# Performance work log

Hardware: AMD Instinct MI355X
Metric: run time of the kernel (lower is better)

The kernel has to match this reference:

```python
import jax, jax.numpy as jnp
import numpy as np

HIDDEN = 512
HEADS = 8
HEAD_DIM = HIDDEN // HEADS
INNER = int(HIDDEN * 4.0)
MAX_DIST = 512
LN_EPS = 1e-5


def _layernorm(x, g, b):
    mu = jnp.mean(x, axis=-1, keepdims=True)
    var = jnp.var(x, axis=-1, keepdims=True)
    return (x - mu) * jax.lax.rsqrt(var + LN_EPS) * g + b


def setup_inputs() -> dict:
    key = jax.random.key(0)
    ks = jax.random.split(key, 12)
    B, T = 4, 2048
    s = 0.02
    return {
        "x": jax.random.normal(ks[0], (B, T, HIDDEN), dtype=jnp.float32),
        "w_qkv": jax.random.normal(ks[1], (HIDDEN, 3 * HIDDEN), dtype=jnp.float32) * s,
        "b_qkv": jnp.zeros((3 * HIDDEN,), dtype=jnp.float32),
        "w_out": jax.random.normal(ks[2], (HIDDEN, HIDDEN), dtype=jnp.float32) * s,
        "b_out": jnp.zeros((HIDDEN,), dtype=jnp.float32),
        "ln1_g": jnp.ones((HIDDEN,), dtype=jnp.float32),
        "ln1_b": jnp.zeros((HIDDEN,), dtype=jnp.float32),
        "ln2_g": jnp.ones((HIDDEN,), dtype=jnp.float32),
        "ln2_b": jnp.zeros((HIDDEN,), dtype=jnp.float32),
        "w_mlp1": jax.random.normal(ks[3], (HIDDEN, INNER), dtype=jnp.float32) * s,
        "b_mlp1": jnp.zeros((INNER,), dtype=jnp.float32),
        "w_mlp2": jax.random.normal(ks[4], (INNER, HIDDEN), dtype=jnp.float32) * s,
        "b_mlp2": jnp.zeros((HIDDEN,), dtype=jnp.float32),
        "rel_table": jax.random.normal(ks[5], (2 * MAX_DIST + 1, HEADS), dtype=jnp.float32) * s,
    }


def reference(x, w_qkv, b_qkv, w_out, b_out, ln1_g, ln1_b, ln2_g, ln2_b,
              w_mlp1, b_mlp1, w_mlp2, b_mlp2, rel_table):
    B, T, C = x.shape
    scale = HEAD_DIM ** -0.5
    qkv = x @ w_qkv + b_qkv  # [B,T,3C]
    qkv = qkv.reshape(B, T, 3, HEADS, HEAD_DIM)
    q = qkv[:, :, 0].transpose(0, 2, 1, 3)  # [B,H,T,D]
    k = qkv[:, :, 1].transpose(0, 2, 1, 3)
    v = qkv[:, :, 2].transpose(0, 2, 1, 3)
    logits = jnp.einsum('bhqd,bhkd->bhqk', q, k) * scale
    # relative position bias: clamp(q_pos - k_pos) lookup -> [H,T,T]
    rel = jnp.clip(jnp.arange(T)[:, None] - jnp.arange(T)[None, :], -MAX_DIST, MAX_DIST) + MAX_DIST
    bias = rel_table[rel].transpose(2, 0, 1)  # [H,T,T]
    logits = logits + bias[None]
    attn = jax.nn.softmax(logits, axis=-1)
    out = jnp.einsum('bhqk,bhkd->bhqd', attn, v)
    out = out.transpose(0, 2, 1, 3).reshape(B, T, C)
    out = out @ w_out + b_out
    x = _layernorm(x + out, ln1_g, ln1_b)
    h = jax.nn.gelu(x @ w_mlp1 + b_mlp1, approximate=False)
    mlp_out = h @ w_mlp2 + b_mlp2
    return _layernorm(x + mlp_out, ln2_g, ln2_b)
```

## Files before the change

kernel.cpp:

```cpp
#include <hip/hip_runtime.h>
#include <hip/hip_bf16.h>

using bf16 = __hip_bfloat16;
typedef __attribute__((ext_vector_type(8))) short bf16x8;
typedef __attribute__((ext_vector_type(4))) short bf16x4;
typedef __attribute__((ext_vector_type(4))) float f32x4;

#define HIDDEN 512
#define HEADS 8
#define HDIM 64
#define INNER 2048
#define MAXD 512
#define BB 4
#define TT 2048
#define MM (BB*TT)
#define LOG2E 1.44269504088896340736f

typedef const __attribute__((address_space(1))) unsigned int* gas_u32p;
typedef __attribute__((address_space(3))) unsigned int* las_u32p;

__device__ __forceinline__ void gload_lds16(const void* g, void* l) {
    __builtin_amdgcn_global_load_lds((gas_u32p)g, (las_u32p)l, 16, 0, 0);
}
__device__ __forceinline__ short bfr(float x) {
    return (short)__bfloat16_as_ushort(__float2bfloat16(x));
}

__global__ __launch_bounds__(256) void cast_kernel(const float* __restrict__ in,
                                                   bf16* __restrict__ out) {
    int i = (blockIdx.x * 256 + threadIdx.x) * 4;
    float4 v = *(const float4*)&in[i];
    bf16 o[4] = {__float2bfloat16(v.x), __float2bfloat16(v.y),
                 __float2bfloat16(v.z), __float2bfloat16(v.w)};
    *(bf16x4*)&out[i] = *(bf16x4*)o;
}

__global__ __launch_bounds__(256) void wtrans_kernel(const float* __restrict__ in,
                                                     bf16* __restrict__ out,
                                                     int K, int N) {
    __shared__ float tile[32][33];
    int bx = blockIdx.x;
    int by = blockIdx.y;
    int lx = threadIdx.x & 31, ly = threadIdx.x >> 5;
    #pragma unroll
    for (int i = 0; i < 4; ++i)
        tile[ly + 8*i][lx] = in[(size_t)(by*32 + ly + 8*i) * N + bx*32 + lx];
    __syncthreads();
    #pragma unroll
    for (int i = 0; i < 4; ++i)
        out[(size_t)(bx*32 + ly + 8*i) * K + by*32 + lx] =
            __float2bfloat16(tile[lx][ly + 8*i]);
}

template<int EPI, int BN, int VT, int RESID>
__global__ __launch_bounds__(256) void gemm_kernel(
    const bf16* __restrict__ A, const bf16* __restrict__ BT,
    const float* __restrict__ bias, const float* __restrict__ resid,
    void* __restrict__ C, bf16* __restrict__ vt_out,
    int M, int N, int K)
{
    constexpr int NBF = BN / 32;
    constexpr int BBYTES = BN * 64;
    __shared__ __align__(16) bf16 As[2][128*32];
    __shared__ __align__(16) bf16 Bs[2][BN*32];
    const int tid = threadIdx.x;
    const int wid = tid >> 6;
    const int lane = tid & 63;
    const int lhi = lane >> 4, llo = lane & 15;
    const int m0 = blockIdx.x * 128, n0 = blockIdx.y * BN;
    const int wr = wid >> 1, wc = wid & 1;

    const int srow = tid >> 2, scol = (tid & 3) * 8;
    const bf16* Ap = A + (size_t)(m0 + srow) * K + scol;
    const bf16* Bp = BT + (size_t)(n0 + srow) * K + scol;
    const size_t step64 = (size_t)64 * K;

    f32x4 acc[4][NBF] = {};

    gload_lds16(Ap,          (char*)As + tid*16);
    gload_lds16(Ap + step64, (char*)As + 4096 + tid*16);
    gload_lds16(Bp,          (char*)Bs + tid*16);
    if (BN == 128) gload_lds16(Bp + step64, (char*)Bs + 4096 + tid*16);

    const int NK = K >> 5;
    for (int it = 0; it < NK; ++it) {
        const int p = it & 1;
        __syncthreads();
        if (it + 1 < NK) {
            const int k1 = (it + 1) << 5;
            gload_lds16(Ap + k1,          (char*)As + (p^1)*8192 + tid*16);
            gload_lds16(Ap + k1 + step64, (char*)As + (p^1)*8192 + 4096 + tid*16);
            gload_lds16(Bp + k1,          (char*)Bs + (p^1)*BBYTES + tid*16);
            if (BN == 128) gload_lds16(Bp + k1 + step64, (char*)Bs + (p^1)*BBYTES + 4096 + tid*16);
        }
        bf16x8 af[4], bfrg[NBF];
        #pragma unroll
        for (int ar = 0; ar < 4; ++ar)
            af[ar] = *(const bf16x8*)((const char*)As + p*8192 + (64*wr + 16*ar + llo)*64 + lhi*16);
        #pragma unroll
        for (int bc = 0; bc < NBF; ++bc)
            bfrg[bc] = *(const bf16x8*)((const char*)Bs + p*BBYTES + ((BN/2)*wc + 16*bc + llo)*64 + lhi*16);
        #pragma unroll
        for (int ar = 0; ar < 4; ++ar)
            #pragma unroll
            for (int bc = 0; bc < NBF; ++bc)
                acc[ar][bc] = __builtin_amdgcn_mfma_f32_16x16x32_bf16(
                    af[ar], bfrg[bc], acc[ar][bc], 0, 0, 0);
    }

    if (VT && n0 >= 1024) {
        #pragma unroll
        for (int ar = 0; ar < 4; ++ar) {
            const int row = m0 + 64*wr + 16*ar + 4*lhi;
            const int bq = row >> 11, t0 = row & 2047;
            #pragma unroll
            for (int bc = 0; bc < NBF; ++bc) {
                const int cv = n0 - 1024 + (BN/2)*wc + 16*bc + llo;
                const int h = cv >> 6, d = cv & 63;
                float bv = bias[n0 + (BN/2)*wc + 16*bc + llo];
                bf16x4 pk = {bfr(acc[ar][bc][0] + bv), bfr(acc[ar][bc][1] + bv),
                             bfr(acc[ar][bc][2] + bv), bfr(acc[ar][bc][3] + bv)};
                *(bf16x4*)&vt_out[(((size_t)(bq*8 + h) * 64 + d) << 11) + t0] = pk;
            }
        }
        return;
    }

    #pragma unroll
    for (int ar = 0; ar < 4; ++ar) {
        #pragma unroll
        for (int j = 0; j < 4; ++j) {
            int row = m0 + 64*wr + 16*ar + 4*lhi + j;
            #pragma unroll
            for (int bc = 0; bc < NBF; ++bc) {
                int col = n0 + (BN/2)*wc + 16*bc + llo;
                float v = acc[ar][bc][j] + bias[col];
                if (RESID) v += resid[(size_t)row * N + col];
                if (EPI == 2) {
                    float u = 0.7978845608028654f * (v + 0.044715f * v * v * v);
                    float e = __builtin_amdgcn_exp2f(u * (2.0f * LOG2E));
                    v = v * (1.0f - 1.0f / (1.0f + e));
                }
                if (EPI == 1)
                    ((float*)C)[(size_t)row * N + col] = v;
                else
                    ((bf16*)C)[(size_t)row * N + col] = __float2bfloat16(v);
            }
        }
    }
}

#define PTN (TT + 128)
__global__ __launch_bounds__(512) void attn_kernel(
    const bf16* __restrict__ qkv,
    const bf16* __restrict__ v_t,
    const float* __restrict__ rel_table,
    bf16* __restrict__ attn_out)
{
    __shared__ __align__(16) bf16 Ks[2][64*64];
    __shared__ __align__(16) bf16 Vs[2][64*64];
    __shared__ __align__(16) bf16 Ps[8][16*64];
    __shared__ float PT[PTN];

    const int qt = blockIdx.x, bh = blockIdx.y;
    const int b = bh >> 3, h = bh & 7;
    const int tid = threadIdx.x, wid = tid >> 6, lane = tid & 63;
    const int lhi = lane >> 4, llo = lane & 15;

    const int lo = qt * 128 - (TT - 1);
    for (int i = tid; i < PTN; i += 512) {
        int idx = min(max(i + lo, -MAXD), MAXD) + MAXD;
        PT[i] = rel_table[(size_t)idx * HEADS + h] * LOG2E;
    }

    const int q0w = qt * 128 + wid * 16;
    const int q = q0w + llo;
    bf16x8 bq[2];
    #pragma unroll
    for (int kc = 0; kc < 2; ++kc)
        bq[kc] = *(const bf16x8*)&qkv[(size_t)(b*TT + q) * 1536 + h*64 + kc*32 + lhi*8];

    const int so = tid * 16;
    const int r0 = so >> 7;
    const int c0 = (((so & 127) ^ ((r0 & 7) << 4)) >> 1);
    const bf16* kbase = qkv + (size_t)(b*TT) * 1536 + 512 + h*64;
    const bf16* vbase = v_t + (size_t)bh * 64 * TT;

    float accL = 0.f;
    f32x4 accO[4] = {};
    const int pti = wid*16 + llo + (TT - 1);

    gload_lds16(kbase + (size_t)r0 * 1536 + c0, (char*)Ks + so);
    gload_lds16(vbase + (size_t)r0 * TT + c0,   (char*)Vs + so);

    constexpr int NT = TT / 64;
    for (int kt = 0; kt < NT; ++kt) {
        const int p = kt & 1;
        const int kv0 = kt * 64;
        __syncthreads();
        if (kt + 1 < NT) {
            const int kn = kv0 + 64;
            gload_lds16(kbase + (size_t)(kn + r0) * 1536 + c0, (char*)Ks + (p^1)*8192 + so);
            gload_lds16(vbase + (size_t)r0 * TT + kn + c0,     (char*)Vs + (p^1)*8192 + so);
        }
        const char* Kb = (const char*)Ks + p*8192;
        const char* Vb = (const char*)Vs + p*8192;

        f32x4 s[4];
        __builtin_amdgcn_s_setprio(1);
        #pragma unroll
        for (int f = 0; f < 4; ++f) {
            f32x4 a = {};
            const int rr = 16*f + llo;
            #pragma unroll
            for (int kc = 0; kc < 2; ++kc) {
                bf16x8 ak = *(const bf16x8*)(Kb + rr*128 + (((4*kc + lhi) ^ (rr & 7)) << 4));
                a = __builtin_amdgcn_mfma_f32_16x16x32_bf16(ak, bq[kc], a, 0, 0, 0);
            }
            s[f] = a;
        }
        __builtin_amdgcn_s_setprio(0);

        const int ib = pti - kv0;
        #pragma unroll
        for (int f = 0; f < 4; ++f)
            #pragma unroll
            for (int j = 0; j < 4; ++j)
                s[f][j] = s[f][j] * (0.125f * LOG2E) + PT[ib - 16*f - 4*lhi - j];
        float tf[4];
        #pragma unroll
        for (int f = 0; f < 4; ++f) {
            float p0 = __builtin_amdgcn_exp2f(s[f][0]);
            float p1 = __builtin_amdgcn_exp2f(s[f][1]);
            float p2 = __builtin_amdgcn_exp2f(s[f][2]);
            float p3 = __builtin_amdgcn_exp2f(s[f][3]);
            tf[f] = (p0 + p1) + (p2 + p3);
            bf16x4 pk = {bfr(p0), bfr(p1), bfr(p2), bfr(p3)};
            *(bf16x4*)((char*)Ps + wid*2048 + llo*128 +
                       ((f*32 + lhi*8) ^ ((llo & 7) << 4))) = pk;
        }
        accL += (tf[0] + tf[1]) + (tf[2] + tf[3]);

        bf16x8 pf[2];
        #pragma unroll
        for (int kc = 0; kc < 2; ++kc)
            pf[kc] = *(const bf16x8*)((const char*)Ps + wid*2048 + llo*128 +
                                      ((kc*64 + lhi*16) ^ ((llo & 7) << 4)));
        __builtin_amdgcn_s_setprio(1);
        #pragma unroll
        for (int kc = 0; kc < 2; ++kc)
            #pragma unroll
            for (int f = 0; f < 4; ++f) {
                const int rr = 16*f + llo;
                bf16x8 av = *(const bf16x8*)(Vb + rr*128 + (((4*kc + lhi) ^ (rr & 7)) << 4));
                accO[f] = __builtin_amdgcn_mfma_f32_16x16x32_bf16(av, pf[kc], accO[f], 0, 0, 0);
            }
        __builtin_amdgcn_s_setprio(0);
    }

    accL += __shfl_xor(accL, 16, 64);
    accL += __shfl_xor(accL, 32, 64);
    const float rl = 1.0f / accL;
    const int row = b*TT + q;
    #pragma unroll
    for (int f = 0; f < 4; ++f) {
        bf16x4 ov = {bfr(accO[f][0] * rl), bfr(accO[f][1] * rl),
                     bfr(accO[f][2] * rl), bfr(accO[f][3] * rl)};
        *(bf16x4*)&attn_out[(size_t)row * HIDDEN + h*64 + 16*f + 4*lhi] = ov;
    }
}

template<int WB>
__global__ __launch_bounds__(256) void ln_kernel(
    const float* __restrict__ in,
    const float* __restrict__ g, const float* __restrict__ bb,
    float* __restrict__ of, bf16* __restrict__ ob)
{
    int row = blockIdx.x * 4 + (threadIdx.x >> 6);
    int lane = threadIdx.x & 63;
    const float* pa = in + (size_t)row * HIDDEN;
    float v[8];
    float s = 0.f, sq = 0.f;
    #pragma unroll
    for (int i = 0; i < 2; ++i) {
        float4 a4 = *(const float4*)&pa[lane*4 + i*256];
        v[i*4+0] = a4.x; v[i*4+1] = a4.y; v[i*4+2] = a4.z; v[i*4+3] = a4.w;
        #pragma unroll
        for (int j = 0; j < 4; ++j) { s += v[i*4+j]; sq += v[i*4+j]*v[i*4+j]; }
    }
    #pragma unroll
    for (int d = 1; d < 64; d <<= 1) {
        s  += __shfl_xor(s,  d, 64);
        sq += __shfl_xor(sq, d, 64);
    }
    float mean = s * (1.f / HIDDEN);
    float var  = sq * (1.f / HIDDEN) - mean * mean;
    float rstd = rsqrtf(var + 1e-5f);
    #pragma unroll
    for (int i = 0; i < 2; ++i)
        #pragma unroll
        for (int j = 0; j < 4; ++j) {
            int col = lane*4 + i*256 + j;
            float o = (v[i*4+j] - mean) * rstd * g[col] + bb[col];
            of[(size_t)row * HIDDEN + col] = o;
            if (WB) ob[(size_t)row * HIDDEN + col] = __float2bfloat16(o);
        }
}

extern "C" void kernel_launch(void* const* d_in, const int* in_sizes, int n_in,
                              void* d_out, int out_size, void* d_ws, size_t ws_size,
                              hipStream_t stream) {
    const float* x     = (const float*)d_in[0];
    const float* w_qkv = (const float*)d_in[1];
    const float* b_qkv = (const float*)d_in[2];
    const float* w_out = (const float*)d_in[3];
    const float* b_out = (const float*)d_in[4];
    const float* ln1_g = (const float*)d_in[5];
    const float* ln1_b = (const float*)d_in[6];
    const float* ln2_g = (const float*)d_in[7];
    const float* ln2_b = (const float*)d_in[8];
    const float* w1    = (const float*)d_in[9];
    const float* b1    = (const float*)d_in[10];
    const float* w2    = (const float*)d_in[11];
    const float* b2    = (const float*)d_in[12];
    const float* rel   = (const float*)d_in[13];
    float* out = (float*)d_out;

    char* ws = (char*)d_ws;
    bf16*  xb     = (bf16*)(ws + 0);
    bf16*  wqkv_t = (bf16*)(ws + 8388608);
    bf16*  wout_t = (bf16*)(ws + 9961472);
    bf16*  w1_t   = (bf16*)(ws + 10485760);
    bf16*  w2_t   = (bf16*)(ws + 12582912);
    bf16*  qkv    = (bf16*)(ws + 14680064);
    bf16*  v_t    = (bf16*)(ws + 39845888);
    bf16*  attn_o = (bf16*)(ws + 48234496);
    float* proj   = (float*)(ws + 56623104);
    float* x1     = (float*)(ws + 73400320);
    bf16*  x1b    = (bf16*)(ws + 90177536);
    bf16*  h      = (bf16*)(ws + 14680064);

    cast_kernel<<<MM*HIDDEN/4/256, 256, 0, stream>>>(x, xb);
    wtrans_kernel<<<dim3(1536/32, 512/32),  256, 0, stream>>>(w_qkv, wqkv_t, 512, 1536);
    wtrans_kernel<<<dim3(512/32,  512/32),  256, 0, stream>>>(w_out, wout_t, 512, 512);
    wtrans_kernel<<<dim3(2048/32, 512/32),  256, 0, stream>>>(w1,    w1_t,   512, 2048);
    wtrans_kernel<<<dim3(512/32,  2048/32), 256, 0, stream>>>(w2,    w2_t,   2048, 512);
    gemm_kernel<0,128,1,0><<<dim3(MM/128, 1536/128), 256, 0, stream>>>(
        xb, wqkv_t, b_qkv, nullptr, qkv, v_t, MM, 1536, 512);
    attn_kernel<<<dim3(TT/128, BB*HEADS), 512, 0, stream>>>(qkv, v_t, rel, attn_o);
    gemm_kernel<1,64,0,1><<<dim3(MM/128, 512/64), 256, 0, stream>>>(
        attn_o, wout_t, b_out, x, proj, nullptr, MM, 512, 512);
    ln_kernel<1><<<MM/4, 256, 0, stream>>>(proj, ln1_g, ln1_b, x1, x1b);
    gemm_kernel<2,128,0,0><<<dim3(MM/128, 2048/128), 256, 0, stream>>>(
        x1b, w1_t, b1, nullptr, h, nullptr, MM, 2048, 512);
    gemm_kernel<1,64,0,1><<<dim3(MM/128, 512/64), 256, 0, stream>>>(
        h, w2_t, b2, x1, proj, nullptr, MM, 512, 2048);
    ln_kernel<0><<<MM/4, 256, 0, stream>>>(proj, ln2_g, ln2_b, out, nullptr);
}
```

Baseline: 195.6 us.

## Swizzle blocks across XCDs, compact bias table, MFMA row sums in attention

Adds an XCD-aware block index swizzle to the GEMM and attention kernels so neighbouring tiles share an L2. The attention kernel now keeps the raw 1025-entry relative-bias table in LDS and picks per key tile between constant far-past and far-future bias values, direct indexing, or clamped indexing. It also computes softmax row sums with an extra MFMA against a ones vector instead of VALU adds plus shuffles, and sets an occupancy hint in launch bounds. The cost is extra branching and one more MFMA per key chunk, plus a dependence on the swizzle being a valid permutation of the grid.

```diff
diff --git a/kernel.cpp b/kernel.cpp
--- a/kernel.cpp
+++ b/kernel.cpp
@@ -24,6 +24,9 @@
 }
 __device__ __forceinline__ short bfr(float x) {
     return (short)__bfloat16_as_ushort(__float2bfloat16(x));
+}
+__device__ __forceinline__ int xcd_swizzle(int bid, int nwg) {
+    return (bid & 7) * (nwg >> 3) + (bid >> 3);
 }
 
 __global__ __launch_bounds__(256) void cast_kernel(const float* __restrict__ in,
@@ -67,7 +70,9 @@
     const int wid = tid >> 6;
     const int lane = tid & 63;
     const int lhi = lane >> 4, llo = lane & 15;
-    const int m0 = blockIdx.x * 128, n0 = blockIdx.y * BN;
+    const int nwg = gridDim.x * gridDim.y;
+    int bid = xcd_swizzle(blockIdx.x + gridDim.x * blockIdx.y, nwg);
+    const int m0 = (bid % gridDim.x) * 128, n0 = (bid / gridDim.x) * BN;
     const int wr = wid >> 1, wc = wid & 1;
 
     const int srow = tid >> 2, scol = (tid & 3) * 8;
@@ -150,8 +155,7 @@
     }
 }
 
-#define PTN (TT + 128)
-__global__ __launch_bounds__(512) void attn_kernel(
+__global__ __launch_bounds__(512, 6) void attn_kernel(
     const bf16* __restrict__ qkv,
     const bf16* __restrict__ v_t,
     const float* __restrict__ rel_table,
@@ -160,18 +164,19 @@
     __shared__ __align__(16) bf16 Ks[2][64*64];
     __shared__ __align__(16) bf16 Vs[2][64*64];
     __shared__ __align__(16) bf16 Ps[8][16*64];
-    __shared__ float PT[PTN];
-
-    const int qt = blockIdx.x, bh = blockIdx.y;
+    __shared__ float PT[2*MAXD + 1];
+
+    int bid = xcd_swizzle(blockIdx.x + gridDim.x * blockIdx.y, gridDim.x * gridDim.y);
+    const int qt = bid & 15, bh = bid >> 4;
     const int b = bh >> 3, h = bh & 7;
     const int tid = threadIdx.x, wid = tid >> 6, lane = tid & 63;
     const int lhi = lane >> 4, llo = lane & 15;
 
-    const int lo = qt * 128 - (TT - 1);
-    for (int i = tid; i < PTN; i += 512) {
-        int idx = min(max(i + lo, -MAXD), MAXD) + MAXD;
-        PT[i] = rel_table[(size_t)idx * HEADS + h] * LOG2E;
-    }
+    for (int i = tid; i < 2*MAXD + 1; i += 512)
+        PT[i] = rel_table[(size_t)i * HEADS + h] * LOG2E;
+    __syncthreads();
+    const float cFut = PT[0];
+    const float cPast = PT[2*MAXD];
 
     const int q0w = qt * 128 + wid * 16;
     const int q = q0w + llo;
@@ -179,6 +184,10 @@
     #pragma unroll
     for (int kc = 0; kc < 2; ++kc)
         bq[kc] = *(const bf16x8*)&qkv[(size_t)(b*TT + q) * 1536 + h*64 + kc*32 + lhi*8];
+
+    bf16x8 aones;
+    #pragma unroll
+    for (int i = 0; i < 8; ++i) aones[i] = (short)0x3F80;
 
     const int so = tid * 16;
     const int r0 = so >> 7;
@@ -186,9 +195,8 @@
     const bf16* kbase = qkv + (size_t)(b*TT) * 1536 + 512 + h*64;
     const bf16* vbase = v_t + (size_t)bh * 64 * TT;
 
-    float accL = 0.f;
     f32x4 accO[4] = {};
-    const int pti = wid*16 + llo + (TT - 1);
+    f32x4 accLf = {};
 
     gload_lds16(kbase + (size_t)r0 * 1536 + c0, (char*)Ks + so);
     gload_lds16(vbase + (size_t)r0 * TT + c0,   (char*)Vs + so);
@@ -221,25 +229,46 @@
         }
         __builtin_amdgcn_s_setprio(0);
 
-        const int ib = pti - kv0;
-        #pragma unroll
-        for (int f = 0; f < 4; ++f)
-            #pragma unroll
-            for (int j = 0; j < 4; ++j)
-                s[f][j] = s[f][j] * (0.125f * LOG2E) + PT[ib - 16*f - 4*lhi - j];
-        float tf[4];
+        const float sc = 0.125f * LOG2E;
+        const int E = q - kv0 + MAXD - 4*lhi;
+        if (kv0 >= q0w + 527) {
+            #pragma unroll
+            for (int f = 0; f < 4; ++f)
+                #pragma unroll
+                for (int j = 0; j < 4; ++j)
+                    s[f][j] = fmaf(s[f][j], sc, cFut);
+        } else if (kv0 <= q0w - 575) {
+            #pragma unroll
+            for (int f = 0; f < 4; ++f)
+                #pragma unroll
+                for (int j = 0; j < 4; ++j)
+                    s[f][j] = fmaf(s[f][j], sc, cPast);
+        } else if (kv0 >= q0w - 497 && kv0 <= q0w + 449) {
+            #pragma unroll
+            for (int f = 0; f < 4; ++f)
+                #pragma unroll
+                for (int j = 0; j < 4; ++j)
+                    s[f][j] = fmaf(s[f][j], sc, PT[E - 16*f - j]);
+        } else {
+            #pragma unroll
+            for (int f = 0; f < 4; ++f)
+                #pragma unroll
+                for (int j = 0; j < 4; ++j) {
+                    int ix = min(max(E - 16*f - j, 0), 2*MAXD);
+                    s[f][j] = fmaf(s[f][j], sc, PT[ix]);
+                }
+        }
+
         #pragma unroll
         for (int f = 0; f < 4; ++f) {
             float p0 = __builtin_amdgcn_exp2f(s[f][0]);
             float p1 = __builtin_amdgcn_exp2f(s[f][1]);
             float p2 = __builtin_amdgcn_exp2f(s[f][2]);
             float p3 = __builtin_amdgcn_exp2f(s[f][3]);
-            tf[f] = (p0 + p1) + (p2 + p3);
             bf16x4 pk = {bfr(p0), bfr(p1), bfr(p2), bfr(p3)};
             *(bf16x4*)((char*)Ps + wid*2048 + llo*128 +
                        ((f*32 + lhi*8) ^ ((llo & 7) << 4))) = pk;
         }
-        accL += (tf[0] + tf[1]) + (tf[2] + tf[3]);
 
         bf16x8 pf[2];
         #pragma unroll
@@ -248,19 +277,19 @@
                                       ((kc*64 + lhi*16) ^ ((llo & 7) << 4)));
         __builtin_amdgcn_s_setprio(1);
         #pragma unroll
-        for (int kc = 0; kc < 2; ++kc)
+        for (int kc = 0; kc < 2; ++kc) {
             #pragma unroll
             for (int f = 0; f < 4; ++f) {
                 const int rr = 16*f + llo;
                 bf16x8 av = *(const bf16x8*)(Vb + rr*128 + (((4*kc + lhi) ^ (rr & 7)) << 4));
                 accO[f] = __builtin_amdgcn_mfma_f32_16x16x32_bf16(av, pf[kc], accO[f], 0, 0, 0);
             }
+            accLf = __builtin_amdgcn_mfma_f32_16x16x32_bf16(aones, pf[kc], accLf, 0, 0, 0);
+        }
         __builtin_amdgcn_s_setprio(0);
     }
 
-    accL += __shfl_xor(accL, 16, 64);
-    accL += __shfl_xor(accL, 32, 64);
-    const float rl = 1.0f / accL;
+    const float rl = 1.0f / accLf[0];
     const int row = b*TT + q;
     #pragma unroll
     for (int f = 0; f < 4; ++f) {
@@ -337,8 +366,8 @@
     bf16*  attn_o = (bf16*)(ws + 48234496);
     float* proj   = (float*)(ws + 56623104);
     float* x1     = (float*)(ws + 73400320);
+    bf16*  h      = (bf16*)(ws + 14680064);
     bf16*  x1b    = (bf16*)(ws + 90177536);
-    bf16*  h      = (bf16*)(ws + 14680064);
 
     cast_kernel<<<MM*HIDDEN/4/256, 256, 0, stream>>>(x, xb);
     wtrans_kernel<<<dim3(1536/32, 512/32),  256, 0, stream>>>(w_qkv, wqkv_t, 512, 1536);
```

After: 221.5 us. 13.2% more time.
